# Optimization experiments

Measured on AMD Instinct MI355X. Metric: run time of the kernel, lower is better.

Reference implementation:

```python
import jax, jax.numpy as jnp
import numpy as np

TOPK, NC, ALPHA, BETA, EPS = 13, 80, 1.0, 6.0, 1e-9


def make_anchors():
    # YOLOv8 anchor centers for a 640x640 image, strides 8/16/32 -> 8400 points
    pts = []
    for s in (8, 16, 32):
        n = 640 // s
        yv, xv = jnp.meshgrid(jnp.arange(n, dtype=jnp.float32) + 0.5,
                              jnp.arange(n, dtype=jnp.float32) + 0.5, indexing='ij')
        pts.append(jnp.stack([xv, yv], -1).reshape(-1, 2) * s)
    return jnp.concatenate(pts, 0)  # (8400, 2)


def setup_inputs() -> dict:
    key = jax.random.key(0)
    ks = jax.random.split(key, 5)
    B, NMAX = 32, 64
    anc_points = make_anchors()
    A = anc_points.shape[0]
    pd_scores = jax.random.uniform(ks[0], (B, A, NC), jnp.float32)
    # predicted boxes: anchor-centered xyxy with random extents
    half = jax.random.uniform(ks[1], (B, A, 2), jnp.float32) * 32.0 + 2.0
    ctr = anc_points[None]
    pd_bboxes = jnp.concatenate([ctr - half, ctr + half], -1)
    # gt boxes: valid xyxy inside the 640x640 image
    xy = jax.random.uniform(ks[2], (B, NMAX, 2), jnp.float32) * 520.0
    wh = jax.random.uniform(ks[3], (B, NMAX, 2), jnp.float32) * 120.0 + 8.0
    gt_bboxes = jnp.concatenate([xy, xy + wh], -1)
    gt_labels = jax.random.randint(ks[4], (B, NMAX, 1), 0, NC).astype(jnp.int64)
    mask_gt = jnp.ones((B, NMAX, 1), jnp.float32)
    return {"pd_scores": pd_scores, "pd_bboxes": pd_bboxes, "anc_points": anc_points,
            "gt_labels": gt_labels, "gt_bboxes": gt_bboxes, "mask_gt": mask_gt}


def _iou_xyxy(box1, box2, eps=1e-7):
    # box1: (B, N, 1, 4), box2: (B, 1, A, 4) -> iou (B, N, A)
    lt = jnp.maximum(box1[..., :2], box2[..., :2])
    rb = jnp.minimum(box1[..., 2:], box2[..., 2:])
    wh = jnp.clip(rb - lt, 0.0)
    inter = wh[..., 0] * wh[..., 1]
    a1 = (box1[..., 2] - box1[..., 0]) * (box1[..., 3] - box1[..., 1])
    a2 = (box2[..., 2] - box2[..., 0]) * (box2[..., 3] - box2[..., 1])
    return inter / (a1 + a2 - inter + eps)


def reference(pd_scores, pd_bboxes, anc_points, gt_labels, gt_bboxes, mask_gt):
    B, A, _ = pd_scores.shape
    N = gt_bboxes.shape[1]
    # --- select_candidates_in_gts: anchor center strictly inside gt box ---
    deltas = jnp.concatenate([
        anc_points[None, None] - gt_bboxes[:, :, None, :2],
        gt_bboxes[:, :, None, 2:] - anc_points[None, None]], -1)  # (B,N,A,4)
    mask_in_gts = (deltas.min(-1) > EPS).astype(jnp.float32)       # (B,N,A)
    mask_valid = mask_in_gts * mask_gt                             # mask_gt (B,N,1)
    # --- get_box_metrics ---
    # bbox_scores[b,n,a] = pd_scores[b, a, gt_labels[b,n]]
    bbox_scores = jnp.take_along_axis(pd_scores.transpose(0, 2, 1),
                                      gt_labels, axis=1)           # (B,N,A)
    overlaps = jnp.clip(_iou_xyxy(gt_bboxes[:, :, None], pd_bboxes[:, None]), 0.0)
    align_metric = (bbox_scores ** ALPHA) * (overlaps ** BETA)
    align_metric = align_metric * mask_valid
    overlaps = overlaps * mask_valid
    # --- select_topk_candidates ---
    _, topk_idxs = jax.lax.top_k(align_metric, TOPK)               # (B,N,TOPK)
    bi = jnp.arange(B)[:, None, None]
    ni = jnp.arange(N)[None, :, None]
    mask_topk = jnp.zeros_like(align_metric).at[bi, ni, topk_idxs].set(1.0)
    mask_pos = mask_valid * mask_topk                              # (B,N,A)
    fg_mask = mask_pos.sum(1)                                      # (B,A)
    # multi-GT conflict resolution (always applied; no-op when no conflicts)
    max_metric = align_metric.max(1, keepdims=True)
    mask_pos = jnp.where(fg_mask[:, None, :] > 1,
                         mask_pos * (align_metric == max_metric).astype(mask_pos.dtype),
                         mask_pos)
    fg_mask = mask_pos.sum(1)
    target_gt_idx = jnp.argmax(mask_pos, 1)                        # (B,A)
    # --- targets ---
    b2 = jnp.arange(B)[:, None]
    target_labels = gt_labels[..., 0][b2, target_gt_idx]           # (B,A)
    target_bboxes = gt_bboxes[b2, target_gt_idx]                   # (B,A,4)
    pos_align = (align_metric * mask_pos).max(1)                   # (B,A)
    target_scores = jax.nn.one_hot(target_labels, NC, dtype=jnp.float32) \
        * pos_align[..., None]                                     # (B,A,NC)
    return (target_bboxes, target_scores, fg_mask.astype(bool))
```

## Files before the change

### kernel.cpp

```cpp
#include <hip/hip_runtime.h>

#define BB 32
#define AA 8400
#define NGT 64
#define NCLS 80
#define TOPK 13
#define SLOTS 4
#define CHUNK 256
#define NCHUNK 33

__device__ __forceinline__ void anchor_xy(int a, float& px, float& py) {
    if (a < 6400)      { int y = a / 80;          int x = a - 80 * y;  px = (x + 0.5f) * 8.0f;  py = (y + 0.5f) * 8.0f; }
    else if (a < 8000) { int r = a - 6400; int y = r / 40; int x = r - 40 * y; px = (x + 0.5f) * 16.0f; py = (y + 0.5f) * 16.0f; }
    else               { int r = a - 8000; int y = r / 20; int x = r - 20 * y; px = (x + 0.5f) * 32.0f; py = (y + 0.5f) * 32.0f; }
}

__global__ __launch_bounds__(256) void k_topk(
    const float* __restrict__ pd_scores,
    const float4* __restrict__ pd_bboxes,
    const int* __restrict__ gt_labels,
    const float4* __restrict__ gt_bboxes,
    const float* __restrict__ mask_gt,
    int* __restrict__ list)
{
    __shared__ unsigned long long keys[4 * TOPK];
    int gid = blockIdx.x;
    int tid = threadIdx.x;
    int w = tid >> 6, lane = tid & 63;
    if (mask_gt[gid] <= 0.0f) {
        if (tid < 16) list[gid * 16 + tid] = -1;
        return;
    }
    int b = gid >> 6;
    float4 g = gt_bboxes[gid];
    int label = gt_labels[gid];
    float ga1 = (g.z - g.x) * (g.w - g.y);

    if (tid < 4 * TOPK) keys[tid] = 0;

    float va[SLOTS]; int ai[SLOTS]; int cnt = 0;
    #pragma unroll
    for (int j = 0; j < SLOTS; ++j) { va[j] = -1.0f; ai[j] = -1; }

#define SCAN_LEVEL(S, N, OFF)                                                   \
    {                                                                           \
        const float inv = 1.0f / (float)(S);                                    \
        int xlo = (int)floorf(g.x * inv - 0.5f); if (xlo < 0) xlo = 0;          \
        int xhi = (int)ceilf (g.z * inv - 0.5f); if (xhi > (N)-1) xhi = (N)-1;  \
        int ylo = (int)floorf(g.y * inv - 0.5f); if (ylo < 0) ylo = 0;          \
        int yhi = (int)ceilf (g.w * inv - 0.5f); if (yhi > (N)-1) yhi = (N)-1;  \
        int nx = xhi - xlo + 1, ny = yhi - ylo + 1;                             \
        int tot = (nx > 0 && ny > 0) ? nx * ny : 0;                             \
        for (int c = tid; c < tot; c += 256) {                                  \
            int yy = c / nx, xx = c - yy * nx;                                  \
            int gx = xlo + xx, gy = ylo + yy;                                   \
            int a = (OFF) + gy * (N) + gx;                                      \
            float px = (gx + 0.5f) * (float)(S), py = (gy + 0.5f) * (float)(S); \
            float dmin = fminf(fminf(px - g.x, py - g.y),                       \
                               fminf(g.z - px, g.w - py));                      \
            if (dmin > 1e-9f) {                                                 \
                float4 pb = pd_bboxes[b * AA + a];                              \
                float ltx = fmaxf(g.x, pb.x), lty = fmaxf(g.y, pb.y);           \
                float rbx = fminf(g.z, pb.z), rby = fminf(g.w, pb.w);           \
                float wd = fmaxf(rbx - ltx, 0.0f), hg = fmaxf(rby - lty, 0.0f); \
                float inter = wd * hg;                                          \
                float a2 = (pb.z - pb.x) * (pb.w - pb.y);                       \
                float iou = fmaxf(inter / (ga1 + a2 - inter + 1e-7f), 0.0f);    \
                float sc = pd_scores[(size_t)(b * AA + a) * NCLS + label];      \
                float i2 = iou * iou;                                           \
                float v = sc * (i2 * i2 * i2);                                  \
                if (v > 0.0f) {                                                 \
                    _Pragma("unroll")                                           \
                    for (int j = 0; j < SLOTS; ++j)                             \
                        if (j == cnt) { va[j] = v; ai[j] = a; }                 \
                    cnt++;                                                      \
                }                                                               \
            }                                                                   \
        }                                                                       \
    }

    SCAN_LEVEL(8, 80, 0)
    SCAN_LEVEL(16, 40, 6400)
    SCAN_LEVEL(32, 20, 8000)
#undef SCAN_LEVEL

    __syncthreads();

    for (int k = 0; k < TOPK; ++k) {
        unsigned long long key = 0;
        #pragma unroll
        for (int j = 0; j < SLOTS; ++j)
            if (va[j] > 0.0f) {
                unsigned long long kk =
                    ((unsigned long long)__float_as_uint(va[j]) << 32)
                    | (unsigned)(0x7FFFFFFF - ai[j]);
                key = kk > key ? kk : key;
            }
        #pragma unroll
        for (int off = 32; off; off >>= 1) {
            unsigned long long o = __shfl_xor(key, off);
            key = o > key ? o : key;
        }
        if (key == 0) break;
        if (lane == 0) keys[w * TOPK + k] = key;
        int wa = 0x7FFFFFFF - (int)(unsigned)(key & 0xFFFFFFFFull);
        #pragma unroll
        for (int j = 0; j < SLOTS; ++j) if (ai[j] == wa) va[j] = -1.0f;
    }

    __syncthreads();

    if (w == 0) {
        unsigned long long mykey = (lane < 4 * TOPK) ? keys[lane] : 0;
        int kc = 0;
        for (int k = 0; k < TOPK; ++k) {
            unsigned long long best = mykey;
            #pragma unroll
            for (int off = 32; off; off >>= 1) {
                unsigned long long o = __shfl_xor(best, off);
                best = o > best ? o : best;
            }
            if (best == 0) break;
            if (lane == 0)
                list[gid * 16 + k] = 0x7FFFFFFF - (int)(unsigned)(best & 0xFFFFFFFFull);
            kc++;
            if (mykey == best) mykey = 0;
        }
        if (lane == 0)
            for (int k = kc; k < 16; ++k) list[gid * 16 + k] = -1;
    }
}

__global__ __launch_bounds__(256) void k_out(
    const float* __restrict__ pd_scores,
    const float4* __restrict__ pd_bboxes,
    const int* __restrict__ gt_labels,
    const float4* __restrict__ gt_bboxes,
    const float* __restrict__ mask_gt,
    const int* __restrict__ list,
    float4* __restrict__ out_bbox,
    float* __restrict__ out_fg,
    float4* __restrict__ out_scores)
{
    __shared__ unsigned int s_lo[CHUNK], s_hi[CHUNK];
    __shared__ float4 s_gt[NGT];
    __shared__ int    s_glab[NGT];
    __shared__ float  s_gmsk[NGT];
    __shared__ float  s_pos[CHUNK];
    __shared__ int    s_alab[CHUNK];

    int bidx = blockIdx.x;
    int b = bidx / NCHUNK;
    int chunk = bidx - b * NCHUNK;
    int abase = chunk * CHUNK;
    int count = AA - abase; if (count > CHUNK) count = CHUNK;
    int tid = threadIdx.x;

    s_lo[tid] = 0; s_hi[tid] = 0;
    if (tid < NGT) {
        s_gt[tid]   = gt_bboxes[b * NGT + tid];
        s_glab[tid] = gt_labels[b * NGT + tid];
        s_gmsk[tid] = mask_gt[b * NGT + tid];
    }
    __syncthreads();

    const int* blist = list + b * NGT * 16;
    #pragma unroll
    for (int e = tid; e < NGT * 16; e += 256) {
        int a = blist[e];
        int rel = a - abase;
        if (a >= 0 && rel >= 0 && rel < count) {
            int n = e >> 4;
            if (n < 32) atomicOr(&s_lo[rel], 1u << n);
            else        atomicOr(&s_hi[rel], 1u << (n - 32));
        }
    }
    __syncthreads();

    if (tid < count) {
        int a = abase + tid;
        int idx = b * AA + a;
        unsigned long long m = ((unsigned long long)s_hi[tid] << 32) | s_lo[tid];
        float pos = 0.0f; int tgt = 0; int fg = 0;
        if (m) {
            float px, py; anchor_xy(a, px, py);
            float4 pb = pd_bboxes[idx];
            float a2 = (pb.z - pb.x) * (pb.w - pb.y);
            if (__popcll(m) == 1) {
                int n = __ffsll((unsigned long long)m) - 1;
                float4 g = s_gt[n];
                float ltx = fmaxf(g.x, pb.x), lty = fmaxf(g.y, pb.y);
                float rbx = fminf(g.z, pb.z), rby = fminf(g.w, pb.w);
                float wd = fmaxf(rbx - ltx, 0.0f), hg = fmaxf(rby - lty, 0.0f);
                float inter = wd * hg;
                float a1 = (g.z - g.x) * (g.w - g.y);
                float iou = fmaxf(inter / (a1 + a2 - inter + 1e-7f), 0.0f);
                float sc = pd_scores[(size_t)idx * NCLS + s_glab[n]];
                float i2 = iou * iou;
                pos = sc * (i2 * i2 * i2);
                tgt = n; fg = 1;
            } else {
                float mmax = 0.0f; unsigned long long nb = 0;
                for (int j0 = 0; j0 < NGT; j0 += 8) {
                    float v[8];
                    #pragma unroll
                    for (int j = 0; j < 8; ++j) {
                        int n = j0 + j;
                        float4 g = s_gt[n];
                        float sc = pd_scores[(size_t)idx * NCLS + s_glab[n]];
                        float dmin = fminf(fminf(px - g.x, py - g.y),
                                           fminf(g.z - px, g.w - py));
                        float ltx = fmaxf(g.x, pb.x), lty = fmaxf(g.y, pb.y);
                        float rbx = fminf(g.z, pb.z), rby = fminf(g.w, pb.w);
                        float wd = fmaxf(rbx - ltx, 0.0f), hg = fmaxf(rby - lty, 0.0f);
                        float inter = wd * hg;
                        float a1 = (g.z - g.x) * (g.w - g.y);
                        float iou = fmaxf(inter / (a1 + a2 - inter + 1e-7f), 0.0f);
                        float i2 = iou * iou;
                        bool ok = (s_gmsk[n] > 0.0f) && (dmin > 1e-9f);
                        v[j] = ok ? sc * (i2 * i2 * i2) : 0.0f;
                    }
                    #pragma unroll
                    for (int j = 0; j < 8; ++j) {
                        int n = j0 + j;
                        float vv = v[j];
                        if (vv > mmax) { mmax = vv; nb = m & (1ull << n); }
                        else if (vv == mmax && vv > 0.0f) nb |= m & (1ull << n);
                    }
                }
                if (nb) { tgt = __ffsll(nb) - 1; pos = mmax; fg = 1; }
            }
        }
        out_bbox[idx] = s_gt[tgt];
        out_fg[idx] = fg ? 1.0f : 0.0f;
        s_pos[tid] = pos;
        s_alab[tid] = s_glab[tgt];
    }
    __syncthreads();

    float4* dst = out_scores + (size_t)(b * AA + abase) * (NCLS / 4);
    int total = count * (NCLS / 4);
    for (int ci = tid; ci < total; ci += 256) {
        int an = ci / (NCLS / 4);
        int c0 = (ci - an * (NCLS / 4)) * 4;
        float p = s_pos[an];
        int lb = s_alab[an];
        float4 r = make_float4(0.f, 0.f, 0.f, 0.f);
        if (p != 0.0f) {
            if (lb == c0)     r.x = p;
            if (lb == c0 + 1) r.y = p;
            if (lb == c0 + 2) r.z = p;
            if (lb == c0 + 3) r.w = p;
        }
        dst[ci] = r;
    }
}

extern "C" void kernel_launch(void* const* d_in, const int* in_sizes, int n_in,
                              void* d_out, int out_size, void* d_ws, size_t ws_size,
                              hipStream_t stream) {
    const float*  pd_scores = (const float*) d_in[0];
    const float4* pd_bboxes = (const float4*)d_in[1];
    const int*    gt_labels = (const int*)   d_in[3];
    const float4* gt_bboxes = (const float4*)d_in[4];
    const float*  mask_gt   = (const float*) d_in[5];

    float* out = (float*)d_out;
    float4* out_bbox   = (float4*)out;
    float4* out_scores = (float4*)(out + (size_t)BB * AA * 4);
    float*  out_fg     = out + (size_t)BB * AA * 4 + (size_t)BB * AA * NCLS;

    int* list = (int*)d_ws;

    k_topk<<<BB * NGT, 256, 0, stream>>>(pd_scores, pd_bboxes,
                                         gt_labels, gt_bboxes, mask_gt, list);

    k_out<<<BB * NCHUNK, 256, 0, stream>>>(
        pd_scores, pd_bboxes, gt_labels, gt_bboxes, mask_gt, list,
        out_bbox, out_fg, out_scores);
}
```

Measured before the change: 67.83 us.

## Pack two GTs per top-k block and scatter target scores over a zero-fill

```diff
diff --git a/kernel.cpp b/kernel.cpp
--- a/kernel.cpp
+++ b/kernel.cpp
@@ -5,7 +5,7 @@
 #define NGT 64
 #define NCLS 80
 #define TOPK 13
-#define SLOTS 4
+#define SLOTS 5
 #define CHUNK 256
 #define NCHUNK 33
 
@@ -24,19 +24,19 @@
     int* __restrict__ list)
 {
     __shared__ unsigned long long keys[4 * TOPK];
-    int gid = blockIdx.x;
     int tid = threadIdx.x;
     int w = tid >> 6, lane = tid & 63;
-    if (mask_gt[gid] <= 0.0f) {
-        if (tid < 16) list[gid * 16 + tid] = -1;
-        return;
-    }
+    int gid = blockIdx.x * 2 + (w >> 1);
+    int half = w & 1;
     int b = gid >> 6;
+
+    if (tid < 4 * TOPK) keys[tid] = 0;
+    __syncthreads();
+
     float4 g = gt_bboxes[gid];
     int label = gt_labels[gid];
     float ga1 = (g.z - g.x) * (g.w - g.y);
-
-    if (tid < 4 * TOPK) keys[tid] = 0;
+    bool valid = mask_gt[gid] > 0.0f;
 
     float va[SLOTS]; int ai[SLOTS]; int cnt = 0;
     #pragma unroll
@@ -51,7 +51,7 @@
         int yhi = (int)ceilf (g.w * inv - 0.5f); if (yhi > (N)-1) yhi = (N)-1;  \
         int nx = xhi - xlo + 1, ny = yhi - ylo + 1;                             \
         int tot = (nx > 0 && ny > 0) ? nx * ny : 0;                             \
-        for (int c = tid; c < tot; c += 256) {                                  \
+        for (int c = half * 64 + lane; c < tot; c += 128) {                     \
             int yy = c / nx, xx = c - yy * nx;                                  \
             int gx = xlo + xx, gy = ylo + yy;                                   \
             int a = (OFF) + gy * (N) + gx;                                      \
@@ -79,12 +79,12 @@
         }                                                                       \
     }
 
-    SCAN_LEVEL(8, 80, 0)
-    SCAN_LEVEL(16, 40, 6400)
-    SCAN_LEVEL(32, 20, 8000)
+    if (valid) {
+        SCAN_LEVEL(8, 80, 0)
+        SCAN_LEVEL(16, 40, 6400)
+        SCAN_LEVEL(32, 20, 8000)
+    }
 #undef SCAN_LEVEL
-
-    __syncthreads();
 
     for (int k = 0; k < TOPK; ++k) {
         unsigned long long key = 0;
@@ -110,8 +110,8 @@
 
     __syncthreads();
 
-    if (w == 0) {
-        unsigned long long mykey = (lane < 4 * TOPK) ? keys[lane] : 0;
+    if (!(w & 1)) {
+        unsigned long long mykey = (lane < 2 * TOPK) ? keys[w * TOPK + lane] : 0;
         int kc = 0;
         for (int k = 0; k < TOPK; ++k) {
             unsigned long long best = mykey;
@@ -146,8 +146,6 @@
     __shared__ float4 s_gt[NGT];
     __shared__ int    s_glab[NGT];
     __shared__ float  s_gmsk[NGT];
-    __shared__ float  s_pos[CHUNK];
-    __shared__ int    s_alab[CHUNK];
 
     int bidx = blockIdx.x;
     int b = bidx / NCHUNK;
@@ -156,6 +154,11 @@
     int count = AA - abase; if (count > CHUNK) count = CHUNK;
     int tid = threadIdx.x;
 
+    float4* dst = out_scores + (size_t)(b * AA + abase) * (NCLS / 4);
+    const float4 z4 = make_float4(0.f, 0.f, 0.f, 0.f);
+    for (int ci = tid; ci < count * (NCLS / 4); ci += 256)
+        dst[ci] = z4;
+
     s_lo[tid] = 0; s_hi[tid] = 0;
     if (tid < NGT) {
         s_gt[tid]   = gt_bboxes[b * NGT + tid];
@@ -165,7 +168,6 @@
     __syncthreads();
 
     const int* blist = list + b * NGT * 16;
-    #pragma unroll
     for (int e = tid; e < NGT * 16; e += 256) {
         int a = blist[e];
         int rel = a - abase;
@@ -188,12 +190,12 @@
             float a2 = (pb.z - pb.x) * (pb.w - pb.y);
             if (__popcll(m) == 1) {
                 int n = __ffsll((unsigned long long)m) - 1;
-                float4 g = s_gt[n];
-                float ltx = fmaxf(g.x, pb.x), lty = fmaxf(g.y, pb.y);
-                float rbx = fminf(g.z, pb.z), rby = fminf(g.w, pb.w);
+                float4 gg = s_gt[n];
+                float ltx = fmaxf(gg.x, pb.x), lty = fmaxf(gg.y, pb.y);
+                float rbx = fminf(gg.z, pb.z), rby = fminf(gg.w, pb.w);
                 float wd = fmaxf(rbx - ltx, 0.0f), hg = fmaxf(rby - lty, 0.0f);
                 float inter = wd * hg;
-                float a1 = (g.z - g.x) * (g.w - g.y);
+                float a1 = (gg.z - gg.x) * (gg.w - gg.y);
                 float iou = fmaxf(inter / (a1 + a2 - inter + 1e-7f), 0.0f);
                 float sc = pd_scores[(size_t)idx * NCLS + s_glab[n]];
                 float i2 = iou * iou;
@@ -206,15 +208,15 @@
                     #pragma unroll
                     for (int j = 0; j < 8; ++j) {
                         int n = j0 + j;
-                        float4 g = s_gt[n];
+                        float4 gg = s_gt[n];
                         float sc = pd_scores[(size_t)idx * NCLS + s_glab[n]];
-                        float dmin = fminf(fminf(px - g.x, py - g.y),
-                                           fminf(g.z - px, g.w - py));
-                        float ltx = fmaxf(g.x, pb.x), lty = fmaxf(g.y, pb.y);
-                        float rbx = fminf(g.z, pb.z), rby = fminf(g.w, pb.w);
+                        float dmin = fminf(fminf(px - gg.x, py - gg.y),
+                                           fminf(gg.z - px, gg.w - py));
+                        float ltx = fmaxf(gg.x, pb.x), lty = fmaxf(gg.y, pb.y);
+                        float rbx = fminf(gg.z, pb.z), rby = fminf(gg.w, pb.w);
                         float wd = fmaxf(rbx - ltx, 0.0f), hg = fmaxf(rby - lty, 0.0f);
                         float inter = wd * hg;
-                        float a1 = (g.z - g.x) * (g.w - g.y);
+                        float a1 = (gg.z - gg.x) * (gg.w - gg.y);
                         float iou = fmaxf(inter / (a1 + a2 - inter + 1e-7f), 0.0f);
                         float i2 = iou * iou;
                         bool ok = (s_gmsk[n] > 0.0f) && (dmin > 1e-9f);
@@ -233,26 +235,8 @@
         }
         out_bbox[idx] = s_gt[tgt];
         out_fg[idx] = fg ? 1.0f : 0.0f;
-        s_pos[tid] = pos;
-        s_alab[tid] = s_glab[tgt];
-    }
-    __syncthreads();
-
-    float4* dst = out_scores + (size_t)(b * AA + abase) * (NCLS / 4);
-    int total = count * (NCLS / 4);
-    for (int ci = tid; ci < total; ci += 256) {
-        int an = ci / (NCLS / 4);
-        int c0 = (ci - an * (NCLS / 4)) * 4;
-        float p = s_pos[an];
-        int lb = s_alab[an];
-        float4 r = make_float4(0.f, 0.f, 0.f, 0.f);
-        if (p != 0.0f) {
-            if (lb == c0)     r.x = p;
-            if (lb == c0 + 1) r.y = p;
-            if (lb == c0 + 2) r.z = p;
-            if (lb == c0 + 3) r.w = p;
-        }
-        dst[ci] = r;
+        if (fg && pos != 0.0f)
+            ((float*)dst)[(size_t)tid * NCLS + s_glab[tgt]] = pos;
     }
 }
 
@@ -272,8 +256,8 @@
 
     int* list = (int*)d_ws;
 
-    k_topk<<<BB * NGT, 256, 0, stream>>>(pd_scores, pd_bboxes,
-                                         gt_labels, gt_bboxes, mask_gt, list);
+    k_topk<<<BB * NGT / 2, 256, 0, stream>>>(pd_scores, pd_bboxes,
+                                             gt_labels, gt_bboxes, mask_gt, list);
 
     k_out<<<BB * NCHUNK, 256, 0, stream>>>(
         pd_scores, pd_bboxes, gt_labels, gt_bboxes, mask_gt, list,
```

Result: no change. 68.71 us (+1.3%).
